# Optimization experiments

Measured on AMD Instinct MI355X. Metric: run time of the kernel, lower is better.

## Reference

```python
import jax, jax.numpy as jnp
import numpy as np

RADIUS = 0.025   # gno_radius
K = 64           # max neighbors per query (cap; in-radius mask applied)
BOX = 0.32       # domain edge length -> ~30 avg neighbors at this density


def _linear_init(key, fan_in, fan_out):
    s = 1.0 / np.sqrt(fan_in)
    return jax.random.uniform(key, (fan_in, fan_out), jnp.float32, -s, s)


def setup_inputs() -> dict:
    key = jax.random.key(0)
    ks = jax.random.split(key, 6)
    N = 16384
    rom_ic = jax.random.uniform(ks[0], (N, 3), jnp.float32) * BOX  # y: source points
    fom_ic = jax.random.uniform(ks[1], (N, 3), jnp.float32) * BOX  # x: query points
    rom_f = jax.random.normal(ks[2], (N, 3), jnp.float32)          # f_y: source features
    # kernel MLP: [3, 128, 256, 3] with GELU between layers
    W1 = _linear_init(ks[3], 3, 128)
    W2 = _linear_init(ks[4], 128, 256)
    W3 = _linear_init(ks[5], 256, 3)
    b1 = jnp.zeros((128,), jnp.float32)
    b2 = jnp.zeros((256,), jnp.float32)
    b3 = jnp.zeros((3,), jnp.float32)
    return {"rom_ic": rom_ic, "fom_ic": fom_ic, "rom_f": rom_f,
            "W1": W1, "b1": b1, "W2": W2, "b2": b2, "W3": W3, "b3": b3}


def _neighbors(y, x):
    # radius neighbor search: for each x_i, up to K nearest y_j with ||y_j-x_i|| <= RADIUS
    d2 = jnp.sum((x[:, None, :] - y[None, :, :]) ** 2, axis=-1)  # [Nx, Ny]
    neg_d2, idx = jax.lax.top_k(-d2, K)                          # K nearest per query
    mask = (-neg_d2) <= RADIUS * RADIUS                          # in-radius mask [Nx, K]
    return idx, mask


def _kernel_mlp(h, W1, b1, W2, b2, W3, b3):
    h = jax.nn.gelu(h @ W1 + b1, approximate=False)
    h = jax.nn.gelu(h @ W2 + b2, approximate=False)
    return h @ W3 + b3


def reference(rom_ic, fom_ic, rom_f, W1, b1, W2, b2, W3, b3):
    idx, mask = _neighbors(rom_ic, fom_ic)              # [Nx,K] int, bool
    rel = rom_ic[idx] - fom_ic[:, None, :]              # [Nx,K,3] gather: y_j - x_i
    k = _kernel_mlp(rel, W1, b1, W2, b2, W3, b3)        # [Nx,K,3]
    vals = k * rom_f[idx]                               # 'linear' transform: k(y-x)*f_y
    m = mask[..., None]
    s = jnp.sum(jnp.where(m, vals, 0.0), axis=1)        # [Nx,3] scatter-sum
    cnt = jnp.sum(mask, axis=1, keepdims=True).astype(s.dtype)
    return s / jnp.maximum(cnt, 1.0)                    # mean over neighbors (0 if none)
```

## Files before the change

### kernel.cpp

```cpp
#include <hip/hip_runtime.h>
#include <math.h>

constexpr float RADIUS = 0.025f;
constexpr float R2 = (float)(0.025 * 0.025);
constexpr int   KMAX = 64;
constexpr float BOX  = 0.32f;
constexpr int   G    = 12;
constexpr int   NCELL = G * G * G;

typedef unsigned short u16;
typedef unsigned int   u32;
typedef unsigned long long u64;
using bf16x8 = __attribute__((ext_vector_type(8))) short;
using f32x4  = __attribute__((ext_vector_type(4))) float;

__device__ __forceinline__ float gelu_l1(float x) {
    float t = x * 0.70710678118654752440f;
    float s = t * t;
    float p =            1.1283791670955126e-01f;
    p = fmaf(p, s, -3.7612638903183754e-01f);
    p = fmaf(p, s,  1.1283791670955126e+00f);
    return 0.5f * x * fmaf(t, p, 1.0f);
}
__device__ __forceinline__ float gelu_l2(float x) {
    float t = x * 0.70710678118654752440f;
    float s = t * t;
    float p =            5.2239776254421878e-03f;
    p = fmaf(p, s, -2.6866170645131252e-02f);
    p = fmaf(p, s,  1.1283791670955126e-01f);
    p = fmaf(p, s, -3.7612638903183754e-01f);
    p = fmaf(p, s,  1.1283791670955126e+00f);
    return 0.5f * x * fmaf(t, p, 1.0f);
}

__device__ __forceinline__ u16 f2bf(float x) {
    u32 u = __float_as_uint(x);
    return (u16)((u + 0x7FFFu + ((u >> 16) & 1u)) >> 16);
}
__device__ __forceinline__ float bf2f(u16 h) {
    return __uint_as_float(((u32)h) << 16);
}
__device__ __forceinline__ int cell_of(float v) {
    int c = (int)(v * ((float)G / BOX));
    return c < 0 ? 0 : (c >= G ? G - 1 : c);
}

__global__ void k_count(const float* __restrict__ y, int n, int* __restrict__ cellCount) {
    int i = blockIdx.x * blockDim.x + threadIdx.x;
    if (i >= n) return;
    int cx = cell_of(y[i * 3 + 0]);
    int cy = cell_of(y[i * 3 + 1]);
    int cz = cell_of(y[i * 3 + 2]);
    atomicAdd(&cellCount[(cz * G + cy) * G + cx], 1);
}

__global__ void k_scan(const int* __restrict__ in, int* __restrict__ out, int n) {
    __shared__ int s[1024];
    int t = threadIdx.x;
    int chunk = (n + 1023) / 1024;
    int lo = t * chunk, hi = min(lo + chunk, n);
    int sum = 0;
    for (int i = lo; i < hi; ++i) sum += in[i];
    s[t] = sum;
    __syncthreads();
    for (int off = 1; off < 1024; off <<= 1) {
        int v = (t >= off) ? s[t - off] : 0;
        __syncthreads();
        s[t] += v;
        __syncthreads();
    }
    int pre = (t == 0) ? 0 : s[t - 1];
    for (int i = lo; i < hi; ++i) { out[i] = pre; pre += in[i]; }
    if (t == 1023) out[n] = s[1023];
}

__global__ void k_scatter(const float* __restrict__ y, int n,
                          const int* __restrict__ cellStart, int* __restrict__ cellFill,
                          float4* __restrict__ sortedP) {
    int i = blockIdx.x * blockDim.x + threadIdx.x;
    if (i >= n) return;
    float px = y[i * 3 + 0], py = y[i * 3 + 1], pz = y[i * 3 + 2];
    int cx = cell_of(px), cy = cell_of(py), cz = cell_of(pz);
    int c = (cz * G + cy) * G + cx;
    int pos = cellStart[c] + atomicAdd(&cellFill[c], 1);
    sortedP[pos] = make_float4(px, py, pz, __int_as_float(i));
}

__global__ __launch_bounds__(512) void k_neighbors(
    const float4* __restrict__ sortedP, const float* __restrict__ x, int nq,
    const int* __restrict__ cellStart,
    int* __restrict__ nbrIdx, float* __restrict__ nbrD2,
    int* __restrict__ cnt) {
    int q = blockIdx.x * 8 + (threadIdx.x >> 6);
    if (q >= nq) return;
    int l = threadIdx.x & 63;
    float qx = x[q * 3 + 0], qy = x[q * 3 + 1], qz = x[q * 3 + 2];
    int cx = cell_of(qx), cy = cell_of(qy), cz = cell_of(qz);
    int c = 0;
    int*   my  = nbrIdx + (size_t)q * KMAX;
    float* myd = nbrD2  + (size_t)q * KMAX;
    u64 below = (1ull << l) - 1ull;

    for (int dz = -1; dz <= 1; ++dz) {
        int z = cz + dz; if (z < 0 || z >= G) continue;
        for (int dy = -1; dy <= 1; ++dy) {
            int yy = cy + dy; if (yy < 0 || yy >= G) continue;
            for (int dx = -1; dx <= 1; ++dx) {
                int xx = cx + dx; if (xx < 0 || xx >= G) continue;
                int cellId = (z * G + yy) * G + xx;
                int s0 = cellStart[cellId], s1 = cellStart[cellId + 1];
                for (int off = s0; off < s1; off += 64) {
                    int u = off + l;
                    bool hit = false;
                    float d2 = 0.f;
                    int j = 0;
                    if (u < s1) {
                        float4 pj = sortedP[u];
                        float ax = pj.x - qx;
                        float ay = pj.y - qy;
                        float az = pj.z - qz;
                        d2 = __fmul_rn(ax, ax);
                        d2 = __fadd_rn(d2, __fmul_rn(ay, ay));
                        d2 = __fadd_rn(d2, __fmul_rn(az, az));
                        hit = (d2 <= R2);
                        j = __float_as_int(pj.w);
                    }
                    u64 m = __ballot(hit);
                    if (hit) {
                        int pos = c + (int)__popcll(m & below);
                        if (pos < KMAX) { my[pos] = j; myd[pos] = d2; }
                    }
                    c += (int)__popcll(m);
                }
            }
        }
    }

    if (c <= KMAX) {
        if (l == 0) cnt[q] = c;
        return;
    }
    if (l == 0) {
        int cc = 0;
        for (int dz = -1; dz <= 1; ++dz) {
            int z = cz + dz; if (z < 0 || z >= G) continue;
            for (int dy = -1; dy <= 1; ++dy) {
                int yy = cy + dy; if (yy < 0 || yy >= G) continue;
                for (int dx = -1; dx <= 1; ++dx) {
                    int xx = cx + dx; if (xx < 0 || xx >= G) continue;
                    int cellId = (z * G + yy) * G + xx;
                    int s0 = cellStart[cellId], s1 = cellStart[cellId + 1];
                    for (int u = s0; u < s1; ++u) {
                        float4 pj = sortedP[u];
                        float ax = pj.x - qx;
                        float ay = pj.y - qy;
                        float az = pj.z - qz;
                        float d2 = __fmul_rn(ax, ax);
                        d2 = __fadd_rn(d2, __fmul_rn(ay, ay));
                        d2 = __fadd_rn(d2, __fmul_rn(az, az));
                        if (d2 <= R2) {
                            int j = __float_as_int(pj.w);
                            if (cc < KMAX) {
                                my[cc] = j; myd[cc] = d2; ++cc;
                            } else {
                                int mi = 0; float md = myd[0];
                                for (int t2 = 1; t2 < KMAX; ++t2) {
                                    float v = myd[t2];
                                    if (v > md) { md = v; mi = t2; }
                                }
                                if (d2 < md) { my[mi] = j; myd[mi] = d2; }
                            }
                        }
                    }
                }
            }
        }
        cnt[q] = cc;
    }
}

__global__ __launch_bounds__(256) void k_build_pairs(
    const int* __restrict__ nbrIdx, const int* __restrict__ cnt,
    const int* __restrict__ qoff, int nq,
    int* __restrict__ pairq, int* __restrict__ pairsrc) {
    int q = blockIdx.x * 4 + (threadIdx.x >> 6);
    if (q >= nq) return;
    int l = threadIdx.x & 63;
    int o = qoff[q], n = cnt[q];
    if (l < n) {
        pairq[o + l]   = q;
        pairsrc[o + l] = nbrIdx[(size_t)q * KMAX + l];
    }
}

__global__ void k_prepw2(const float* __restrict__ W2, u16* __restrict__ Whi, u16* __restrict__ Wlo,
                         const float* __restrict__ b2, const float* __restrict__ W3,
                         float4* __restrict__ b2w3) {
    int idx = blockIdx.x * blockDim.x + threadIdx.x;
    if (idx >= 128 * 256) return;
    int k = idx >> 8, n = idx & 255;
    float v = W2[idx];
    u16 hi = f2bf(v);
    u16 lo = f2bf(v - bf2f(hi));
    Whi[n * 128 + k] = hi;
    Wlo[n * 128 + k] = lo;
    if (idx < 256) {
        b2w3[idx] = make_float4(b2[idx], W3[idx * 3 + 0], W3[idx * 3 + 1], W3[idx * 3 + 2]);
    }
}

__global__ __launch_bounds__(512, 4) void k_mlp(
    const float* __restrict__ y, const float* __restrict__ x,
    const int* __restrict__ pairq, const int* __restrict__ pairsrc,
    const int* __restrict__ qoff, int nq,
    const float* __restrict__ W1, const float* __restrict__ b1,
    const u16* __restrict__ W2Thi, const u16* __restrict__ W2Tlo,
    const float4* __restrict__ b2w3, const float* __restrict__ b3,
    float* __restrict__ kvals)
{
    __shared__ float relS[128][4];
    __shared__ u16 Ahi[4 * 8 * 64 * 8];
    __shared__ u16 Alo[4 * 8 * 64 * 8];

    int P = qoff[nq];
    int base = blockIdx.x * 128;
    if (base >= P) return;
    int t = threadIdx.x;
    int w = t >> 6, l = t & 63;

    if (t < 128) {
        int pi = base + t;
        float r0 = 0.f, r1 = 0.f, r2 = 0.f;
        if (pi < P) {
            int q = pairq[pi], s = pairsrc[pi];
            r0 = y[s * 3 + 0] - x[q * 3 + 0];
            r1 = y[s * 3 + 1] - x[q * 3 + 1];
            r2 = y[s * 3 + 2] - x[q * 3 + 2];
        }
        relS[t][0] = r0; relS[t][1] = r1; relS[t][2] = r2;
    }
    __syncthreads();

    int ksw = w & 3;
    int pg  = w >> 2;

    {
        int p = pg * 64 + l;
        float r0 = relS[p][0], r1 = relS[p][1], r2 = relS[p][2];
        int pb = p >> 4, i = p & 15;
        bf16x8 hv, lv;
        #pragma unroll
        for (int kk = 0; kk < 32; ++kk) {
            int k = ksw * 32 + kk;
            float h = b1[k] + r0 * W1[k] + r1 * W1[128 + k] + r2 * W1[256 + k];
            float g = gelu_l1(h);
            u32 gb = __float_as_uint(g);
            float ghi = __uint_as_float(gb & 0xFFFF0000u);
            hv[kk & 7] = (short)(gb >> 16);
            lv[kk & 7] = (short)f2bf(g - ghi);
            if ((kk & 7) == 7) {
                int slot = i + 16 * (kk >> 3);
                int off = ((ksw * 8 + pb) * 64 + slot) * 8;
                *(bf16x8*)&Ahi[off] = hv;
                *(bf16x8*)&Alo[off] = lv;
            }
        }
    }
    __syncthreads();

    f32x4 acc[8][2];
    #pragma unroll
    for (int pb = 0; pb < 8; ++pb)
        #pragma unroll
        for (int ub = 0; ub < 2; ++ub)
            acc[pb][ub] = f32x4{0.f, 0.f, 0.f, 0.f};

    int col = l & 15, krow = l >> 4;
    #pragma unroll
    for (int ks = 0; ks < 4; ++ks) {
        bf16x8 bh[2], bl[2];
        #pragma unroll
        for (int ub = 0; ub < 2; ++ub) {
            int n = w * 32 + ub * 16 + col;
            size_t off = (size_t)n * 128 + ks * 32 + krow * 8;
            bh[ub] = *(const bf16x8*)(W2Thi + off);
            bl[ub] = *(const bf16x8*)(W2Tlo + off);
        }
        #pragma unroll
        for (int pb = 0; pb < 8; ++pb) {
            int off = ((ks * 8 + pb) * 64 + l) * 8;
            bf16x8 ah = *(const bf16x8*)&Ahi[off];
            bf16x8 al = *(const bf16x8*)&Alo[off];
            #pragma unroll
            for (int ub = 0; ub < 2; ++ub) {
                acc[pb][ub] = __builtin_amdgcn_mfma_f32_16x16x32_bf16(bh[ub], ah, acc[pb][ub], 0, 0, 0);
                acc[pb][ub] = __builtin_amdgcn_mfma_f32_16x16x32_bf16(bl[ub], ah, acc[pb][ub], 0, 0, 0);
                acc[pb][ub] = __builtin_amdgcn_mfma_f32_16x16x32_bf16(bh[ub], al, acc[pb][ub], 0, 0, 0);
            }
        }
    }
    __syncthreads();

    float (*red)[128][3] = (float (*)[128][3])Alo;

    #pragma unroll
    for (int pb = 0; pb < 8; ++pb) {
        float pc0 = 0.f, pc1 = 0.f, pc2 = 0.f;
        #pragma unroll
        for (int ub = 0; ub < 2; ++ub)
            #pragma unroll
            for (int r = 0; r < 4; ++r) {
                int unit = w * 32 + ub * 16 + krow * 4 + r;
                float4 bw = b2w3[unit];
                float g = gelu_l2(acc[pb][ub][r] + bw.x);
                pc0 += g * bw.y;
                pc1 += g * bw.z;
                pc2 += g * bw.w;
            }
        pc0 += __shfl_xor(pc0, 16, 64);
        pc1 += __shfl_xor(pc1, 16, 64);
        pc2 += __shfl_xor(pc2, 16, 64);
        pc0 += __shfl_xor(pc0, 32, 64);
        pc1 += __shfl_xor(pc1, 32, 64);
        pc2 += __shfl_xor(pc2, 32, 64);
        if (krow == 0) {
            int pair = pb * 16 + col;
            red[w][pair][0] = pc0;
            red[w][pair][1] = pc1;
            red[w][pair][2] = pc2;
        }
    }
    __syncthreads();
    if (t < 384) {
        int p = t / 3, c = t % 3;
        float v = b3[c] + red[0][p][c] + red[1][p][c] + red[2][p][c] + red[3][p][c]
                        + red[4][p][c] + red[5][p][c] + red[6][p][c] + red[7][p][c];
        if (base + p < P) kvals[(size_t)(base + p) * 3 + c] = v;
    }
}

__global__ __launch_bounds__(256) void k_finalize(
    const float* __restrict__ kvals, const int* __restrict__ pairsrc,
    const float* __restrict__ f, const int* __restrict__ qoff,
    const int* __restrict__ cnt, int nq, float* __restrict__ out) {
    int q = blockIdx.x * 4 + (threadIdx.x >> 6);
    if (q >= nq) return;
    int l = threadIdx.x & 63;
    int o = qoff[q], n = cnt[q];
    float s0 = 0.f, s1 = 0.f, s2 = 0.f;
    if (l < n) {
        int src = pairsrc[o + l];
        s0 = kvals[(size_t)(o + l) * 3 + 0] * f[src * 3 + 0];
        s1 = kvals[(size_t)(o + l) * 3 + 1] * f[src * 3 + 1];
        s2 = kvals[(size_t)(o + l) * 3 + 2] * f[src * 3 + 2];
    }
    #pragma unroll
    for (int off = 1; off < 64; off <<= 1) {
        s0 += __shfl_xor(s0, off, 64);
        s1 += __shfl_xor(s1, off, 64);
        s2 += __shfl_xor(s2, off, 64);
    }
    if (l == 0) {
        float d = (n > 0) ? (float)n : 1.0f;
        out[q * 3 + 0] = s0 / d;
        out[q * 3 + 1] = s1 / d;
        out[q * 3 + 2] = s2 / d;
    }
}

extern "C" void kernel_launch(void* const* d_in, const int* in_sizes, int n_in,
                              void* d_out, int out_size, void* d_ws, size_t ws_size,
                              hipStream_t stream) {
    const float* rom_ic = (const float*)d_in[0];
    const float* fom_ic = (const float*)d_in[1];
    const float* rom_f  = (const float*)d_in[2];
    const float* W1 = (const float*)d_in[3];
    const float* b1 = (const float*)d_in[4];
    const float* W2 = (const float*)d_in[5];
    const float* b2 = (const float*)d_in[6];
    const float* W3 = (const float*)d_in[7];
    const float* b3 = (const float*)d_in[8];
    float* out = (float*)d_out;

    int n  = in_sizes[0] / 3;
    int nq = in_sizes[1] / 3;

    char* p = (char*)d_ws;
    auto alloc = [&](size_t bytes) -> void* {
        void* r = (void*)p;
        p += (bytes + 255) & ~(size_t)255;
        return r;
    };
    int*    cellCount = (int*)alloc(NCELL * 4);
    int*    cellFill  = (int*)alloc(NCELL * 4);
    int*    cellStart = (int*)alloc((NCELL + 1) * 4);
    float4* sortedP   = (float4*)alloc((size_t)n * 16);
    int*    nbrIdx    = (int*)alloc((size_t)nq * KMAX * 4);
    float*  nbrD2     = (float*)alloc((size_t)nq * KMAX * 4);
    int*    cnt       = (int*)alloc((size_t)nq * 4);
    int*    qoff      = (int*)alloc(((size_t)nq + 1) * 4);
    int*    pairq     = (int*)alloc((size_t)nq * KMAX * 4);
    int*    pairsrc   = (int*)alloc((size_t)nq * KMAX * 4);
    float*  kvals     = (float*)alloc((size_t)nq * KMAX * 3 * 4);
    u16*    W2Thi     = (u16*)alloc(128 * 256 * 2);
    u16*    W2Tlo     = (u16*)alloc(128 * 256 * 2);
    float4* b2w3      = (float4*)alloc(256 * 16);

    hipMemsetAsync(cellCount, 0, NCELL * 4, stream);
    hipMemsetAsync(cellFill,  0, NCELL * 4, stream);

    int blocksN  = (n + 255) / 256;

    k_count<<<blocksN, 256, 0, stream>>>(rom_ic, n, cellCount);
    k_scan<<<1, 1024, 0, stream>>>(cellCount, cellStart, NCELL);
    k_scatter<<<blocksN, 256, 0, stream>>>(rom_ic, n, cellStart, cellFill, sortedP);
    k_prepw2<<<128, 256, 0, stream>>>(W2, W2Thi, W2Tlo, b2, W3, b2w3);
    k_neighbors<<<(nq + 7) / 8, 512, 0, stream>>>(sortedP, fom_ic, nq, cellStart,
                                                  nbrIdx, nbrD2, cnt);
    k_scan<<<1, 1024, 0, stream>>>(cnt, qoff, nq);
    k_build_pairs<<<(nq + 3) / 4, 256, 0, stream>>>(nbrIdx, cnt, qoff, nq, pairq, pairsrc);
    k_mlp<<<(nq + 1) / 2, 512, 0, stream>>>(rom_ic, fom_ic, pairq, pairsrc, qoff, nq,
                                            W1, b1, W2Thi, W2Tlo, b2w3, b3, kvals);
    k_finalize<<<(nq + 3) / 4, 256, 0, stream>>>(kvals, pairsrc, rom_f, qoff, cnt, nq, out);
}
```

Measured before the change: 255.8 us.

## Fuse pair compaction into neighbor search via atomic offset allocation

The neighbor kernel now keeps each query's neighbor list in shared memory and reserves its slice of the compacted pair array with one atomicAdd per wave, writing pairq and pairsrc directly. This drops the separate scan and build-pairs kernels and the global nbrIdx/nbrD2 round trip. In exchange, pair order across queries becomes nondeterministic. k_finalize still reads qoff and cnt, so it stays correct as long as it does not assume contiguous ordering.

Measured after the change: 397.6 us. +55.5%, slower.

```diff
diff --git a/kernel.cpp b/kernel.cpp
--- a/kernel.cpp
+++ b/kernel.cpp
@@ -89,16 +89,17 @@
 __global__ __launch_bounds__(512) void k_neighbors(
     const float4* __restrict__ sortedP, const float* __restrict__ x, int nq,
     const int* __restrict__ cellStart,
-    int* __restrict__ nbrIdx, float* __restrict__ nbrD2,
-    int* __restrict__ cnt) {
-    int q = blockIdx.x * 8 + (threadIdx.x >> 6);
+    int* __restrict__ pairq, int* __restrict__ pairsrc,
+    int* __restrict__ qoff, int* __restrict__ cnt, int* __restrict__ totalPairs) {
+    __shared__ int   nbrS[8][KMAX];
+    __shared__ float d2S[8][KMAX];
+    int wv = threadIdx.x >> 6;
+    int q = blockIdx.x * 8 + wv;
     if (q >= nq) return;
     int l = threadIdx.x & 63;
     float qx = x[q * 3 + 0], qy = x[q * 3 + 1], qz = x[q * 3 + 2];
     int cx = cell_of(qx), cy = cell_of(qy), cz = cell_of(qz);
     int c = 0;
-    int*   my  = nbrIdx + (size_t)q * KMAX;
-    float* myd = nbrD2  + (size_t)q * KMAX;
     u64 below = (1ull << l) - 1ull;
 
     for (int dz = -1; dz <= 1; ++dz) {
@@ -128,7 +129,7 @@
                     u64 m = __ballot(hit);
                     if (hit) {
                         int pos = c + (int)__popcll(m & below);
-                        if (pos < KMAX) { my[pos] = j; myd[pos] = d2; }
+                        if (pos < KMAX) nbrS[wv][pos] = j;
                     }
                     c += (int)__popcll(m);
                 }
@@ -136,61 +137,55 @@
         }
     }
 
-    if (c <= KMAX) {
-        if (l == 0) cnt[q] = c;
-        return;
-    }
-    if (l == 0) {
-        int cc = 0;
-        for (int dz = -1; dz <= 1; ++dz) {
-            int z = cz + dz; if (z < 0 || z >= G) continue;
-            for (int dy = -1; dy <= 1; ++dy) {
-                int yy = cy + dy; if (yy < 0 || yy >= G) continue;
-                for (int dx = -1; dx <= 1; ++dx) {
-                    int xx = cx + dx; if (xx < 0 || xx >= G) continue;
-                    int cellId = (z * G + yy) * G + xx;
-                    int s0 = cellStart[cellId], s1 = cellStart[cellId + 1];
-                    for (int u = s0; u < s1; ++u) {
-                        float4 pj = sortedP[u];
-                        float ax = pj.x - qx;
-                        float ay = pj.y - qy;
-                        float az = pj.z - qz;
-                        float d2 = __fmul_rn(ax, ax);
-                        d2 = __fadd_rn(d2, __fmul_rn(ay, ay));
-                        d2 = __fadd_rn(d2, __fmul_rn(az, az));
-                        if (d2 <= R2) {
-                            int j = __float_as_int(pj.w);
-                            if (cc < KMAX) {
-                                my[cc] = j; myd[cc] = d2; ++cc;
-                            } else {
-                                int mi = 0; float md = myd[0];
-                                for (int t2 = 1; t2 < KMAX; ++t2) {
-                                    float v = myd[t2];
-                                    if (v > md) { md = v; mi = t2; }
+    int cc = (c <= KMAX) ? c : KMAX;
+    if (c > KMAX) {
+        if (l == 0) {
+            int k2 = 0;
+            for (int dz = -1; dz <= 1; ++dz) {
+                int z = cz + dz; if (z < 0 || z >= G) continue;
+                for (int dy = -1; dy <= 1; ++dy) {
+                    int yy = cy + dy; if (yy < 0 || yy >= G) continue;
+                    for (int dx = -1; dx <= 1; ++dx) {
+                        int xx = cx + dx; if (xx < 0 || xx >= G) continue;
+                        int cellId = (z * G + yy) * G + xx;
+                        int s0 = cellStart[cellId], s1 = cellStart[cellId + 1];
+                        for (int u = s0; u < s1; ++u) {
+                            float4 pj = sortedP[u];
+                            float ax = pj.x - qx;
+                            float ay = pj.y - qy;
+                            float az = pj.z - qz;
+                            float d2 = __fmul_rn(ax, ax);
+                            d2 = __fadd_rn(d2, __fmul_rn(ay, ay));
+                            d2 = __fadd_rn(d2, __fmul_rn(az, az));
+                            if (d2 <= R2) {
+                                int j = __float_as_int(pj.w);
+                                if (k2 < KMAX) {
+                                    nbrS[wv][k2] = j; d2S[wv][k2] = d2; ++k2;
+                                } else {
+                                    int mi = 0; float md = d2S[wv][0];
+                                    for (int t2 = 1; t2 < KMAX; ++t2) {
+                                        float v = d2S[wv][t2];
+                                        if (v > md) { md = v; mi = t2; }
+                                    }
+                                    if (d2 < md) { nbrS[wv][mi] = j; d2S[wv][mi] = d2; }
                                 }
-                                if (d2 < md) { my[mi] = j; myd[mi] = d2; }
                             }
                         }
                     }
                 }
             }
         }
-        cnt[q] = cc;
-    }
-}
-
-__global__ __launch_bounds__(256) void k_build_pairs(
-    const int* __restrict__ nbrIdx, const int* __restrict__ cnt,
-    const int* __restrict__ qoff, int nq,
-    int* __restrict__ pairq, int* __restrict__ pairsrc) {
-    int q = blockIdx.x * 4 + (threadIdx.x >> 6);
-    if (q >= nq) return;
-    int l = threadIdx.x & 63;
-    int o = qoff[q], n = cnt[q];
-    if (l < n) {
-        pairq[o + l]   = q;
-        pairsrc[o + l] = nbrIdx[(size_t)q * KMAX + l];
-    }
+    }
+    __builtin_amdgcn_wave_barrier();
+
+    int base = 0;
+    if (l == 0) base = atomicAdd(totalPairs, cc);
+    base = __shfl(base, 0, 64);
+    if (l < cc) {
+        pairq[base + l]   = q;
+        pairsrc[base + l] = nbrS[wv][l];
+    }
+    if (l == 0) { qoff[q] = base; cnt[q] = cc; }
 }
 
 __global__ void k_prepw2(const float* __restrict__ W2, u16* __restrict__ Whi, u16* __restrict__ Wlo,
@@ -212,7 +207,7 @@
 __global__ __launch_bounds__(512, 4) void k_mlp(
     const float* __restrict__ y, const float* __restrict__ x,
     const int* __restrict__ pairq, const int* __restrict__ pairsrc,
-    const int* __restrict__ qoff, int nq,
+    const int* __restrict__ totalPairs, int nq,
     const float* __restrict__ W1, const float* __restrict__ b1,
     const u16* __restrict__ W2Thi, const u16* __restrict__ W2Tlo,
     const float4* __restrict__ b2w3, const float* __restrict__ b3,
@@ -222,7 +217,7 @@
     __shared__ u16 Ahi[4 * 8 * 64 * 8];
     __shared__ u16 Alo[4 * 8 * 64 * 8];
 
-    int P = qoff[nq];
+    int P = *totalPairs;
     int base = blockIdx.x * 128;
     if (base >= P) return;
     int t = threadIdx.x;
@@ -391,35 +386,33 @@
         p += (bytes + 255) & ~(size_t)255;
         return r;
     };
-    int*    cellCount = (int*)alloc(NCELL * 4);
-    int*    cellFill  = (int*)alloc(NCELL * 4);
-    int*    cellStart = (int*)alloc((NCELL + 1) * 4);
-    float4* sortedP   = (float4*)alloc((size_t)n * 16);
-    int*    nbrIdx    = (int*)alloc((size_t)nq * KMAX * 4);
-    float*  nbrD2     = (float*)alloc((size_t)nq * KMAX * 4);
-    int*    cnt       = (int*)alloc((size_t)nq * 4);
-    int*    qoff      = (int*)alloc(((size_t)nq + 1) * 4);
-    int*    pairq     = (int*)alloc((size_t)nq * KMAX * 4);
-    int*    pairsrc   = (int*)alloc((size_t)nq * KMAX * 4);
-    float*  kvals     = (float*)alloc((size_t)nq * KMAX * 3 * 4);
-    u16*    W2Thi     = (u16*)alloc(128 * 256 * 2);
-    u16*    W2Tlo     = (u16*)alloc(128 * 256 * 2);
-    float4* b2w3      = (float4*)alloc(256 * 16);
+    int*    cellCount  = (int*)alloc(NCELL * 4);
+    int*    cellFill   = (int*)alloc(NCELL * 4);
+    int*    cellStart  = (int*)alloc((NCELL + 1) * 4);
+    float4* sortedP    = (float4*)alloc((size_t)n * 16);
+    int*    cnt        = (int*)alloc((size_t)nq * 4);
+    int*    qoff       = (int*)alloc((size_t)nq * 4);
+    int*    pairq      = (int*)alloc((size_t)nq * KMAX * 4);
+    int*    pairsrc    = (int*)alloc((size_t)nq * KMAX * 4);
+    float*  kvals      = (float*)alloc((size_t)nq * KMAX * 3 * 4);
+    u16*    W2Thi      = (u16*)alloc(128 * 256 * 2);
+    u16*    W2Tlo      = (u16*)alloc(128 * 256 * 2);
+    float4* b2w3       = (float4*)alloc(256 * 16);
+    int*    totalPairs = (int*)alloc(256);
 
     hipMemsetAsync(cellCount, 0, NCELL * 4, stream);
     hipMemsetAsync(cellFill,  0, NCELL * 4, stream);
-
-    int blocksN  = (n + 255) / 256;
+    hipMemsetAsync(totalPairs, 0, 4, stream);
+
+    int blocksN = (n + 255) / 256;
 
     k_count<<<blocksN, 256, 0, stream>>>(rom_ic, n, cellCount);
     k_scan<<<1, 1024, 0, stream>>>(cellCount, cellStart, NCELL);
     k_scatter<<<blocksN, 256, 0, stream>>>(rom_ic, n, cellStart, cellFill, sortedP);
     k_prepw2<<<128, 256, 0, stream>>>(W2, W2Thi, W2Tlo, b2, W3, b2w3);
     k_neighbors<<<(nq + 7) / 8, 512, 0, stream>>>(sortedP, fom_ic, nq, cellStart,
-                                                  nbrIdx, nbrD2, cnt);
-    k_scan<<<1, 1024, 0, stream>>>(cnt, qoff, nq);
-    k_build_pairs<<<(nq + 3) / 4, 256, 0, stream>>>(nbrIdx, cnt, qoff, nq, pairq, pairsrc);
-    k_mlp<<<(nq + 1) / 2, 512, 0, stream>>>(rom_ic, fom_ic, pairq, pairsrc, qoff, nq,
+                                                  pairq, pairsrc, qoff, cnt, totalPairs);
+    k_mlp<<<(nq + 1) / 2, 512, 0, stream>>>(rom_ic, fom_ic, pairq, pairsrc, totalPairs, nq,
                                             W1, b1, W2Thi, W2Tlo, b2w3, b3, kvals);
     k_finalize<<<(nq + 3) / 4, 256, 0, stream>>>(kvals, pairsrc, rom_f, qoff, cnt, nq, out);
 }
```
